# Kernel optimization log

Hardware: AMD Instinct MI355X
Metric: run time of the kernel (lower is better)

## Reference

```python
import jax, jax.numpy as jnp
import numpy as np

N, E = 50000, 800000
DIN, H, R, HEADS, DH, OUT = 256, 128, 8, 8, 16, 3  # DH = H // HEADS


def setup_inputs() -> dict:
    key = jax.random.key(0)
    ks = jax.random.split(key, 16)
    g = lambda k, shape, fan: jax.random.normal(k, shape, jnp.float32) * np.float32(np.sqrt(2.0 / fan))
    return {
        'x': jax.random.normal(ks[0], (N, DIN), jnp.float32),
        'edge_index': jax.random.randint(ks[1], (2, E), 0, N, jnp.int32),
        'edge_type': jax.random.randint(ks[2], (E,), 0, R, jnp.int32),
        'Wp': g(ks[3], (DIN, H), DIN), 'bp': jnp.zeros((H,), jnp.float32),
        'W1': g(ks[4], (R, H, H), H), 'root1': g(ks[5], (H, H), H), 'b1': jnp.zeros((H,), jnp.float32),
        'W2': g(ks[6], (R, H, H), H), 'root2': g(ks[7], (H, H), H), 'b2': jnp.zeros((H,), jnp.float32),
        'Wg': g(ks[8], (H, HEADS * DH), H), 'att': g(ks[9], (1, HEADS, 2 * DH), 2 * DH),
        'bg': jnp.zeros((HEADS * DH,), jnp.float32),
        'Wf': g(ks[10], (H, OUT), H), 'bf': jnp.zeros((OUT,), jnp.float32),
    }


def _rgcn(h, src, tgt, etype, W, root, b):
    # h: [N,H]; per-relation: mean-aggregate W_r @ h_src over edges of type r
    n = h.shape[0]
    h_src = h[src]                                   # [E,H]
    out = h @ root
    for r in range(R):
        mask = (etype == r)
        msg = jnp.where(mask[:, None], h_src @ W[r], 0.0)          # [E,H]
        agg = jax.ops.segment_sum(msg, tgt, num_segments=n)        # [N,H]
        deg = jax.ops.segment_sum(mask.astype(h.dtype), tgt, num_segments=n)
        out = out + agg / jnp.clip(deg, 1.0)[:, None]
    return out + b


def _gat(h, src, tgt, Wg, att, bg, negative_slope=0.2):
    n = h.shape[0]
    z = (h @ Wg).reshape(n, HEADS, DH)               # [N,heads,dh]
    z_src, z_tgt = z[src], z[tgt]                    # [E,heads,dh]
    alpha = (z_src * att[:, :, :DH]).sum(-1) + (z_tgt * att[:, :, DH:]).sum(-1)  # [E,heads]
    alpha = jax.nn.leaky_relu(alpha, negative_slope)
    amax = jax.ops.segment_max(alpha, tgt, num_segments=n)         # [N,heads]
    ex = jnp.exp(alpha - amax[tgt])
    denom = jnp.clip(jax.ops.segment_sum(ex, tgt, num_segments=n), 1e-16)
    alpha = ex / denom[tgt]
    out = jax.ops.segment_sum(z_src * alpha[:, :, None], tgt, num_segments=n)  # [N,heads,dh]
    return out.reshape(n, HEADS * DH) + bg


def reference(x, edge_index, edge_type, Wp, bp, W1, root1, b1, W2, root2, b2, Wg, att, bg, Wf, bf):
    src, tgt = edge_index[0], edge_index[1]
    h = x @ Wp + bp
    h = jax.nn.relu(_rgcn(h, src, tgt, edge_type, W1, root1, b1))
    h = jax.nn.relu(_rgcn(h, src, tgt, edge_type, W2, root2, b2))
    h = _gat(h, src, tgt, Wg, att, bg)
    logits = h @ Wf + bf
    return jax.nn.log_softmax(logits, axis=-1)
```

## Files before the change

kernel.cpp:

```cpp
#include <hip/hip_runtime.h>
#include <math.h>

#define NN      50000
#define EE      800000
#define DIN     256
#define HF      128
#define RR      8
#define NHEADS  8
#define DHH     16
#define OUTC    3
#define M2      (NN * RR)
#define NB2     ((M2 + 255) / 256)
#define CH2     ((NB2 + 255) / 256)

static inline int cdiv(long long a, int b) { return (int)((a + b - 1) / b); }

typedef __attribute__((ext_vector_type(8))) short short8;
typedef __attribute__((ext_vector_type(4))) float f32x4;

__device__ inline float bf2f(unsigned short u) {
    return __uint_as_float(((unsigned)u) << 16);
}
__device__ inline unsigned short f2bf(float f) {
    unsigned u = __float_as_uint(f);
    u += 0x7fffu + ((u >> 16) & 1u);
    return (unsigned short)(u >> 16);
}

__global__ __launch_bounds__(256) void prep_weights(const float* __restrict__ Wp,
                                                    const float* __restrict__ W1,
                                                    const float* __restrict__ root1,
                                                    const float* __restrict__ W2,
                                                    const float* __restrict__ root2,
                                                    const float* __restrict__ Wg,
                                                    unsigned short* __restrict__ Wtp_hi,
                                                    unsigned short* __restrict__ Wtp_lo,
                                                    unsigned short* __restrict__ Wt1_hi,
                                                    unsigned short* __restrict__ Wt1_lo,
                                                    unsigned short* __restrict__ Wt2_hi,
                                                    unsigned short* __restrict__ Wt2_lo,
                                                    unsigned short* __restrict__ Wtg_hi,
                                                    unsigned short* __restrict__ Wtg_lo) {
    int i = blockIdx.x * 256 + threadIdx.x;
    if (i >= 344064) return;
    const float* src; unsigned short *dh, *dl; int k0, ldk, base;
    if (i < 32768)       { src = Wp;    dh = Wtp_hi; dl = Wtp_lo; k0 = 0;    ldk = 256;  base = 0; }
    else if (i < 163840) { src = W1;    dh = Wt1_hi; dl = Wt1_lo; k0 = 0;    ldk = 1152; base = 32768; }
    else if (i < 180224) { src = root1; dh = Wt1_hi; dl = Wt1_lo; k0 = 1024; ldk = 1152; base = 163840; }
    else if (i < 311296) { src = W2;    dh = Wt2_hi; dl = Wt2_lo; k0 = 0;    ldk = 1152; base = 180224; }
    else if (i < 327680) { src = root2; dh = Wt2_hi; dl = Wt2_lo; k0 = 1024; ldk = 1152; base = 311296; }
    else                 { src = Wg;    dh = Wtg_hi; dl = Wtg_lo; k0 = 0;    ldk = 128;  base = 327680; }
    int j = i - base;
    int k = j >> 7, n = j & 127;
    float f = src[(size_t)k * 128 + n];
    unsigned short hi = f2bf(f);
    unsigned short lo = f2bf(f - bf2f(hi));
    dh[(size_t)n * ldk + k0 + k] = hi;
    dl[(size_t)n * ldk + k0 + k] = lo;
}

__global__ __launch_bounds__(256) void count2_kernel(const int* __restrict__ tgt,
                                                     const int* __restrict__ et,
                                                     int* __restrict__ cnt2) {
    int i = blockIdx.x * 256 + threadIdx.x;
    if (i < EE) atomicAdd(&cnt2[tgt[i] * RR + et[i]], 1);
}

__global__ __launch_bounds__(256) void scan1_kernel(const int* __restrict__ cnt,
                                                    int* __restrict__ bsum, int n) {
    __shared__ int s[256];
    int t = threadIdx.x;
    int i = blockIdx.x * 256 + t;
    s[t] = (i < n) ? cnt[i] : 0;
    __syncthreads();
    for (int off = 128; off > 0; off >>= 1) {
        if (t < off) s[t] += s[t + off];
        __syncthreads();
    }
    if (t == 0) bsum[blockIdx.x] = s[0];
}

__global__ __launch_bounds__(256) void scan2_kernel(const int* __restrict__ bsum,
                                                    int* __restrict__ bbase,
                                                    int* __restrict__ tail,
                                                    int nb, int ch) {
    __shared__ int s[256];
    int t = threadIdx.x;
    int beg = t * ch;
    int end = beg + ch; if (end > nb) end = nb;
    int sum = 0;
    for (int i = beg; i < end; i++) sum += bsum[i];
    s[t] = sum;
    __syncthreads();
    for (int off = 1; off < 256; off <<= 1) {
        int u = (t >= off) ? s[t - off] : 0;
        __syncthreads();
        s[t] += u;
        __syncthreads();
    }
    int run = s[t] - sum;
    for (int i = beg; i < end; i++) {
        bbase[i] = run;
        run += bsum[i];
    }
    if (t == 255) *tail = s[255];
}

__global__ __launch_bounds__(256) void scan3_kernel(const int* __restrict__ cnt,
                                                    const int* __restrict__ bbase,
                                                    int* __restrict__ rowptr,
                                                    int* __restrict__ cursor, int n) {
    __shared__ int s[256];
    int t = threadIdx.x;
    int i = blockIdx.x * 256 + t;
    int v = (i < n) ? cnt[i] : 0;
    s[t] = v;
    __syncthreads();
    for (int off = 1; off < 256; off <<= 1) {
        int u = (t >= off) ? s[t - off] : 0;
        __syncthreads();
        s[t] += u;
        __syncthreads();
    }
    if (i < n) {
        int e = bbase[blockIdx.x] + s[t] - v;
        rowptr[i] = e;
        cursor[i] = e;
    }
}

__global__ __launch_bounds__(256) void fill2_kernel(const int* __restrict__ src,
                                                    const int* __restrict__ tgt,
                                                    const int* __restrict__ et,
                                                    int* __restrict__ cursor2,
                                                    int* __restrict__ csr_src2) {
    int e = blockIdx.x * 256 + threadIdx.x;
    if (e >= EE) return;
    int pos = atomicAdd(&cursor2[tgt[e] * RR + et[e]], 1);
    csr_src2[pos] = src[e];
}

#define BK 32
#define APAD 36

template <bool SPLITA, bool ACC, bool BIAS, bool RELU, bool BF16OUT>
__global__ __launch_bounds__(256) void gemm_mfma(const void* __restrict__ Av, int lda,
                                                 const unsigned short* __restrict__ Bthi,
                                                 const unsigned short* __restrict__ Btlo, int ldk,
                                                 float* __restrict__ C,
                                                 unsigned short* __restrict__ Cb,
                                                 const float* __restrict__ bias,
                                                 int M, int K) {
    __shared__ unsigned short Ah[128 * APAD];
    __shared__ unsigned short Al[(SPLITA ? 128 : 1) * APAD];
    __shared__ unsigned short Bh[128 * APAD];
    __shared__ unsigned short Bl[128 * APAD];
    const int tid  = threadIdx.x;
    const int m0   = blockIdx.x * 128;
    const int w    = tid >> 6;
    const int lane = tid & 63;
    const int lrow = lane & 15;
    const int q    = lane >> 4;

    f32x4 acc[2][8];
#pragma unroll
    for (int t = 0; t < 2; t++)
#pragma unroll
        for (int c = 0; c < 8; c++) acc[t][c] = (f32x4){0.f, 0.f, 0.f, 0.f};

    const int srow  = tid >> 1;
    const int spart = (tid & 1) * 16;

    for (int k0 = 0; k0 < K; k0 += BK) {
        if (SPLITA) {
            const float* A = (const float*)Av;
            int gm = m0 + srow;
            float va[16];
            if (gm < M) {
                const float* ap = &A[(size_t)gm * lda + k0 + spart];
#pragma unroll
                for (int j = 0; j < 4; j++) {
                    float4 v = *reinterpret_cast<const float4*>(ap + j * 4);
                    va[j * 4 + 0] = v.x; va[j * 4 + 1] = v.y; va[j * 4 + 2] = v.z; va[j * 4 + 3] = v.w;
                }
            } else {
#pragma unroll
                for (int j = 0; j < 16; j++) va[j] = 0.f;
            }
            unsigned hw[8], lw[8];
#pragma unroll
            for (int j = 0; j < 8; j++) {
                unsigned short h0 = f2bf(va[2 * j]);
                unsigned short h1 = f2bf(va[2 * j + 1]);
                unsigned short l0 = f2bf(va[2 * j] - bf2f(h0));
                unsigned short l1 = f2bf(va[2 * j + 1] - bf2f(h1));
                hw[j] = (unsigned)h0 | ((unsigned)h1 << 16);
                lw[j] = (unsigned)l0 | ((unsigned)l1 << 16);
            }
            *reinterpret_cast<uint4*>(&Ah[srow * APAD + spart])     = make_uint4(hw[0], hw[1], hw[2], hw[3]);
            *reinterpret_cast<uint4*>(&Ah[srow * APAD + spart + 8]) = make_uint4(hw[4], hw[5], hw[6], hw[7]);
            *reinterpret_cast<uint4*>(&Al[srow * APAD + spart])     = make_uint4(lw[0], lw[1], lw[2], lw[3]);
            *reinterpret_cast<uint4*>(&Al[srow * APAD + spart + 8]) = make_uint4(lw[4], lw[5], lw[6], lw[7]);
        } else {
            const unsigned short* A = (const unsigned short*)Av;
            int gm = m0 + srow;
            uint4 v  = make_uint4(0u, 0u, 0u, 0u);
            uint4 v2 = make_uint4(0u, 0u, 0u, 0u);
            if (gm < M) {
                const unsigned short* ap = &A[(size_t)gm * lda + k0 + spart];
                v  = *reinterpret_cast<const uint4*>(ap);
                v2 = *reinterpret_cast<const uint4*>(ap + 8);
            }
            *reinterpret_cast<uint4*>(&Ah[srow * APAD + spart])     = v;
            *reinterpret_cast<uint4*>(&Ah[srow * APAD + spart + 8]) = v2;
        }
        {
            const unsigned short* bh = &Bthi[(size_t)srow * ldk + k0 + spart];
            const unsigned short* bl = &Btlo[(size_t)srow * ldk + k0 + spart];
            *reinterpret_cast<uint4*>(&Bh[srow * APAD + spart])     = *reinterpret_cast<const uint4*>(bh);
            *reinterpret_cast<uint4*>(&Bh[srow * APAD + spart + 8]) = *reinterpret_cast<const uint4*>(bh + 8);
            *reinterpret_cast<uint4*>(&Bl[srow * APAD + spart])     = *reinterpret_cast<const uint4*>(bl);
            *reinterpret_cast<uint4*>(&Bl[srow * APAD + spart + 8]) = *reinterpret_cast<const uint4*>(bl + 8);
        }
        __syncthreads();

        short8 ah[2], al[2];
#pragma unroll
        for (int t = 0; t < 2; t++) {
            ah[t] = *reinterpret_cast<const short8*>(&Ah[(w * 32 + t * 16 + lrow) * APAD + q * 8]);
            if (SPLITA)
                al[t] = *reinterpret_cast<const short8*>(&Al[(w * 32 + t * 16 + lrow) * APAD + q * 8]);
        }
#pragma unroll
        for (int c = 0; c < 8; c++) {
            short8 bh = *reinterpret_cast<const short8*>(&Bh[(c * 16 + lrow) * APAD + q * 8]);
            short8 bl = *reinterpret_cast<const short8*>(&Bl[(c * 16 + lrow) * APAD + q * 8]);
#pragma unroll
            for (int t = 0; t < 2; t++) {
                acc[t][c] = __builtin_amdgcn_mfma_f32_16x16x32_bf16(ah[t], bl, acc[t][c], 0, 0, 0);
                if (SPLITA)
                    acc[t][c] = __builtin_amdgcn_mfma_f32_16x16x32_bf16(al[t], bh, acc[t][c], 0, 0, 0);
                acc[t][c] = __builtin_amdgcn_mfma_f32_16x16x32_bf16(ah[t], bh, acc[t][c], 0, 0, 0);
            }
        }
        __syncthreads();
    }

#pragma unroll
    for (int t = 0; t < 2; t++) {
#pragma unroll
        for (int r = 0; r < 4; r++) {
            int gm = m0 + w * 32 + t * 16 + q * 4 + r;
            if (gm >= M) continue;
#pragma unroll
            for (int c = 0; c < 8; c++) {
                int gn = c * 16 + lrow;
                float v = acc[t][c][r];
                if (BIAS) v += bias[gn];
                if (ACC)  v += C[(size_t)gm * HF + gn];
                if (RELU) v = fmaxf(v, 0.f);
                C[(size_t)gm * HF + gn] = v;
                if (BF16OUT) Cb[(size_t)gm * HF + gn] = f2bf(v);
            }
        }
    }
}

__global__ __launch_bounds__(256) void gemm_rgcn(const unsigned short* __restrict__ aggb,
                                                 const float* __restrict__ hin,
                                                 const unsigned short* __restrict__ Bthi,
                                                 const unsigned short* __restrict__ Btlo,
                                                 float* __restrict__ hout,
                                                 unsigned short* __restrict__ hbout,
                                                 const float* __restrict__ bias, int M) {
    const int LDK = (RR + 1) * HF;
    __shared__ unsigned short Ah[128 * APAD];
    __shared__ unsigned short Al[128 * APAD];
    __shared__ unsigned short Bh[128 * APAD];
    __shared__ unsigned short Bl[128 * APAD];
    const int tid  = threadIdx.x;
    const int m0   = blockIdx.x * 128;
    const int w    = tid >> 6;
    const int lane = tid & 63;
    const int lrow = lane & 15;
    const int q    = lane >> 4;

    f32x4 acc[2][8];
#pragma unroll
    for (int t = 0; t < 2; t++)
#pragma unroll
        for (int c = 0; c < 8; c++) acc[t][c] = (f32x4){0.f, 0.f, 0.f, 0.f};

    const int srow  = tid >> 1;
    const int spart = (tid & 1) * 16;

    for (int k0 = 0; k0 < RR * HF; k0 += BK) {
        {
            int gm = m0 + srow;
            uint4 v  = make_uint4(0u, 0u, 0u, 0u);
            uint4 v2 = make_uint4(0u, 0u, 0u, 0u);
            if (gm < M) {
                const unsigned short* ap = &aggb[(size_t)gm * (RR * HF) + k0 + spart];
                v  = *reinterpret_cast<const uint4*>(ap);
                v2 = *reinterpret_cast<const uint4*>(ap + 8);
            }
            *reinterpret_cast<uint4*>(&Ah[srow * APAD + spart])     = v;
            *reinterpret_cast<uint4*>(&Ah[srow * APAD + spart + 8]) = v2;
        }
        {
            const unsigned short* bh = &Bthi[(size_t)srow * LDK + k0 + spart];
            const unsigned short* bl = &Btlo[(size_t)srow * LDK + k0 + spart];
            *reinterpret_cast<uint4*>(&Bh[srow * APAD + spart])     = *reinterpret_cast<const uint4*>(bh);
            *reinterpret_cast<uint4*>(&Bh[srow * APAD + spart + 8]) = *reinterpret_cast<const uint4*>(bh + 8);
            *reinterpret_cast<uint4*>(&Bl[srow * APAD + spart])     = *reinterpret_cast<const uint4*>(bl);
            *reinterpret_cast<uint4*>(&Bl[srow * APAD + spart + 8]) = *reinterpret_cast<const uint4*>(bl + 8);
        }
        __syncthreads();
        short8 ah[2];
#pragma unroll
        for (int t = 0; t < 2; t++)
            ah[t] = *reinterpret_cast<const short8*>(&Ah[(w * 32 + t * 16 + lrow) * APAD + q * 8]);
#pragma unroll
        for (int c = 0; c < 8; c++) {
            short8 bh = *reinterpret_cast<const short8*>(&Bh[(c * 16 + lrow) * APAD + q * 8]);
            short8 bl = *reinterpret_cast<const short8*>(&Bl[(c * 16 + lrow) * APAD + q * 8]);
#pragma unroll
            for (int t = 0; t < 2; t++) {
                acc[t][c] = __builtin_amdgcn_mfma_f32_16x16x32_bf16(ah[t], bl, acc[t][c], 0, 0, 0);
                acc[t][c] = __builtin_amdgcn_mfma_f32_16x16x32_bf16(ah[t], bh, acc[t][c], 0, 0, 0);
            }
        }
        __syncthreads();
    }

    for (int k0 = 0; k0 < HF; k0 += BK) {
        {
            int gm = m0 + srow;
            float va[16];
            if (gm < M) {
                const float* ap = &hin[(size_t)gm * HF + k0 + spart];
#pragma unroll
                for (int j = 0; j < 4; j++) {
                    float4 v = *reinterpret_cast<const float4*>(ap + j * 4);
                    va[j * 4 + 0] = v.x; va[j * 4 + 1] = v.y; va[j * 4 + 2] = v.z; va[j * 4 + 3] = v.w;
                }
            } else {
#pragma unroll
                for (int j = 0; j < 16; j++) va[j] = 0.f;
            }
            unsigned hw[8], lw[8];
#pragma unroll
            for (int j = 0; j < 8; j++) {
                unsigned short h0 = f2bf(va[2 * j]);
                unsigned short h1 = f2bf(va[2 * j + 1]);
                unsigned short l0 = f2bf(va[2 * j] - bf2f(h0));
                unsigned short l1 = f2bf(va[2 * j + 1] - bf2f(h1));
                hw[j] = (unsigned)h0 | ((unsigned)h1 << 16);
                lw[j] = (unsigned)l0 | ((unsigned)l1 << 16);
            }
            *reinterpret_cast<uint4*>(&Ah[srow * APAD + spart])     = make_uint4(hw[0], hw[1], hw[2], hw[3]);
            *reinterpret_cast<uint4*>(&Ah[srow * APAD + spart + 8]) = make_uint4(hw[4], hw[5], hw[6], hw[7]);
            *reinterpret_cast<uint4*>(&Al[srow * APAD + spart])     = make_uint4(lw[0], lw[1], lw[2], lw[3]);
            *reinterpret_cast<uint4*>(&Al[srow * APAD + spart + 8]) = make_uint4(lw[4], lw[5], lw[6], lw[7]);
        }
        {
            const unsigned short* bh = &Bthi[(size_t)srow * LDK + RR * HF + k0 + spart];
            const unsigned short* bl = &Btlo[(size_t)srow * LDK + RR * HF + k0 + spart];
            *reinterpret_cast<uint4*>(&Bh[srow * APAD + spart])     = *reinterpret_cast<const uint4*>(bh);
            *reinterpret_cast<uint4*>(&Bh[srow * APAD + spart + 8]) = *reinterpret_cast<const uint4*>(bh + 8);
            *reinterpret_cast<uint4*>(&Bl[srow * APAD + spart])     = *reinterpret_cast<const uint4*>(bl);
            *reinterpret_cast<uint4*>(&Bl[srow * APAD + spart + 8]) = *reinterpret_cast<const uint4*>(bl + 8);
        }
        __syncthreads();
        short8 ah[2], al[2];
#pragma unroll
        for (int t = 0; t < 2; t++) {
            ah[t] = *reinterpret_cast<const short8*>(&Ah[(w * 32 + t * 16 + lrow) * APAD + q * 8]);
            al[t] = *reinterpret_cast<const short8*>(&Al[(w * 32 + t * 16 + lrow) * APAD + q * 8]);
        }
#pragma unroll
        for (int c = 0; c < 8; c++) {
            short8 bh = *reinterpret_cast<const short8*>(&Bh[(c * 16 + lrow) * APAD + q * 8]);
            short8 bl = *reinterpret_cast<const short8*>(&Bl[(c * 16 + lrow) * APAD + q * 8]);
#pragma unroll
            for (int t = 0; t < 2; t++) {
                acc[t][c] = __builtin_amdgcn_mfma_f32_16x16x32_bf16(ah[t], bl, acc[t][c], 0, 0, 0);
                acc[t][c] = __builtin_amdgcn_mfma_f32_16x16x32_bf16(al[t], bh, acc[t][c], 0, 0, 0);
                acc[t][c] = __builtin_amdgcn_mfma_f32_16x16x32_bf16(ah[t], bh, acc[t][c], 0, 0, 0);
            }
        }
        __syncthreads();
    }

#pragma unroll
    for (int t = 0; t < 2; t++) {
#pragma unroll
        for (int r = 0; r < 4; r++) {
            int gm = m0 + w * 32 + t * 16 + q * 4 + r;
            if (gm >= M) continue;
#pragma unroll
            for (int c = 0; c < 8; c++) {
                int gn = c * 16 + lrow;
                float v = fmaxf(acc[t][c][r] + bias[gn], 0.f);
                hout[(size_t)gm * HF + gn] = v;
                hbout[(size_t)gm * HF + gn] = f2bf(v);
            }
        }
    }
}

__global__ __launch_bounds__(256) void gemm_z(const float* __restrict__ hin,
                                              const unsigned short* __restrict__ Bthi,
                                              const unsigned short* __restrict__ Btlo,
                                              const float* __restrict__ att,
                                              unsigned short* __restrict__ zb,
                                              float* __restrict__ a_src,
                                              float* __restrict__ a_tgt, int M) {
    __shared__ unsigned short Ah[128 * APAD];
    __shared__ unsigned short Al[128 * APAD];
    __shared__ unsigned short Bh[128 * APAD];
    __shared__ unsigned short Bl[128 * APAD];
    const int tid  = threadIdx.x;
    const int m0   = blockIdx.x * 128;
    const int w    = tid >> 6;
    const int lane = tid & 63;
    const int lrow = lane & 15;
    const int q    = lane >> 4;

    f32x4 acc[2][8];
#pragma unroll
    for (int t = 0; t < 2; t++)
#pragma unroll
        for (int c = 0; c < 8; c++) acc[t][c] = (f32x4){0.f, 0.f, 0.f, 0.f};

    const int srow  = tid >> 1;
    const int spart = (tid & 1) * 16;

    for (int k0 = 0; k0 < HF; k0 += BK) {
        {
            int gm = m0 + srow;
            float va[16];
            if (gm < M) {
                const float* ap = &hin[(size_t)gm * HF + k0 + spart];
#pragma unroll
                for (int j = 0; j < 4; j++) {
                    float4 v = *reinterpret_cast<const float4*>(ap + j * 4);
                    va[j * 4 + 0] = v.x; va[j * 4 + 1] = v.y; va[j * 4 + 2] = v.z; va[j * 4 + 3] = v.w;
                }
            } else {
#pragma unroll
                for (int j = 0; j < 16; j++) va[j] = 0.f;
            }
            unsigned hw[8], lw[8];
#pragma unroll
            for (int j = 0; j < 8; j++) {
                unsigned short h0 = f2bf(va[2 * j]);
                unsigned short h1 = f2bf(va[2 * j + 1]);
                unsigned short l0 = f2bf(va[2 * j] - bf2f(h0));
                unsigned short l1 = f2bf(va[2 * j + 1] - bf2f(h1));
                hw[j] = (unsigned)h0 | ((unsigned)h1 << 16);
                lw[j] = (unsigned)l0 | ((unsigned)l1 << 16);
            }
            *reinterpret_cast<uint4*>(&Ah[srow * APAD + spart])     = make_uint4(hw[0], hw[1], hw[2], hw[3]);
            *reinterpret_cast<uint4*>(&Ah[srow * APAD + spart + 8]) = make_uint4(hw[4], hw[5], hw[6], hw[7]);
            *reinterpret_cast<uint4*>(&Al[srow * APAD + spart])     = make_uint4(lw[0], lw[1], lw[2], lw[3]);
            *reinterpret_cast<uint4*>(&Al[srow * APAD + spart + 8]) = make_uint4(lw[4], lw[5], lw[6], lw[7]);
        }
        {
            const unsigned short* bh = &Bthi[(size_t)srow * HF + k0 + spart];
            const unsigned short* bl = &Btlo[(size_t)srow * HF + k0 + spart];
            *reinterpret_cast<uint4*>(&Bh[srow * APAD + spart])     = *reinterpret_cast<const uint4*>(bh);
            *reinterpret_cast<uint4*>(&Bh[srow * APAD + spart + 8]) = *reinterpret_cast<const uint4*>(bh + 8);
            *reinterpret_cast<uint4*>(&Bl[srow * APAD + spart])     = *reinterpret_cast<const uint4*>(bl);
            *reinterpret_cast<uint4*>(&Bl[srow * APAD + spart + 8]) = *reinterpret_cast<const uint4*>(bl + 8);
        }
        __syncthreads();
        short8 ah[2], al[2];
#pragma unroll
        for (int t = 0; t < 2; t++) {
            ah[t] = *reinterpret_cast<const short8*>(&Ah[(w * 32 + t * 16 + lrow) * APAD + q * 8]);
            al[t] = *reinterpret_cast<const short8*>(&Al[(w * 32 + t * 16 + lrow) * APAD + q * 8]);
        }
#pragma unroll
        for (int c = 0; c < 8; c++) {
            short8 bh = *reinterpret_cast<const short8*>(&Bh[(c * 16 + lrow) * APAD + q * 8]);
            short8 bl = *reinterpret_cast<const short8*>(&Bl[(c * 16 + lrow) * APAD + q * 8]);
#pragma unroll
            for (int t = 0; t < 2; t++) {
                acc[t][c] = __builtin_amdgcn_mfma_f32_16x16x32_bf16(ah[t], bl, acc[t][c], 0, 0, 0);
                acc[t][c] = __builtin_amdgcn_mfma_f32_16x16x32_bf16(al[t], bh, acc[t][c], 0, 0, 0);
                acc[t][c] = __builtin_amdgcn_mfma_f32_16x16x32_bf16(ah[t], bh, acc[t][c], 0, 0, 0);
            }
        }
        __syncthreads();
    }

    float att_s[8], att_t[8];
#pragma unroll
    for (int c = 0; c < 8; c++) {
        att_s[c] = att[c * 32 + lrow];
        att_t[c] = att[c * 32 + 16 + lrow];
    }

#pragma unroll
    for (int t = 0; t < 2; t++) {
#pragma unroll
        for (int r = 0; r < 4; r++) {
            int gm = m0 + w * 32 + t * 16 + q * 4 + r;
            if (gm >= M) continue;
#pragma unroll
            for (int c = 0; c < 8; c++) {
                int gn = c * 16 + lrow;
                float v = acc[t][c][r];
                zb[(size_t)gm * HF + gn] = f2bf(v);
                float ps = v * att_s[c];
                float pt = v * att_t[c];
#pragma unroll
                for (int off = 1; off < 16; off <<= 1) {
                    ps += __shfl_xor(ps, off);
                    pt += __shfl_xor(pt, off);
                }
                if (lrow == 0) {
                    a_src[(size_t)gm * NHEADS + c] = ps;
                    a_tgt[(size_t)gm * NHEADS + c] = pt;
                }
            }
        }
    }
}

__global__ __launch_bounds__(256) void rgcn_agg_sorted(const unsigned short* __restrict__ hb,
                                                       const int* __restrict__ rowptr2,
                                                       const int* __restrict__ csr_src2,
                                                       unsigned short* __restrict__ agg) {
    int w = (blockIdx.x * 256 + threadIdx.x) >> 6;
    if (w >= NN) return;
    int lane = threadIdx.x & 63;
    int half = lane >> 5;
    int c4 = (lane & 31) * 4;
    const int b8 = w * RR;
    unsigned short* o = &agg[(size_t)w * (RR * HF)];
    int b = rowptr2[b8];
#pragma unroll
    for (int r = 0; r < RR; r++) {
        int e2 = rowptr2[b8 + r + 1];
        float a0 = 0.f, a1 = 0.f, a2 = 0.f, a3 = 0.f;
        for (int e = b + half; e < e2; e += 2) {
            int s = csr_src2[e];
            uint2 v = *reinterpret_cast<const uint2*>(&hb[(size_t)s * HF + c4]);
            a0 += bf2f((unsigned short)(v.x & 0xffffu));
            a1 += bf2f((unsigned short)(v.x >> 16));
            a2 += bf2f((unsigned short)(v.y & 0xffffu));
            a3 += bf2f((unsigned short)(v.y >> 16));
        }
        a0 += __shfl_xor(a0, 32);
        a1 += __shfl_xor(a1, 32);
        a2 += __shfl_xor(a2, 32);
        a3 += __shfl_xor(a3, 32);
        int n = e2 - b;
        float inv = 1.f / (float)(n > 1 ? n : 1);
        if (half == 0) {
            uint2 p;
            p.x = (unsigned)f2bf(a0 * inv) | ((unsigned)f2bf(a1 * inv) << 16);
            p.y = (unsigned)f2bf(a2 * inv) | ((unsigned)f2bf(a3 * inv) << 16);
            *reinterpret_cast<uint2*>(&o[r * HF + c4]) = p;
        }
        b = e2;
    }
}

__global__ __launch_bounds__(256) void gat_kernel(const int* __restrict__ rowptr2,
                                                  const int* __restrict__ csr_src2,
                                                  const float* __restrict__ a_src,
                                                  const float* __restrict__ a_tgt,
                                                  const unsigned short* __restrict__ zb,
                                                  const float* __restrict__ bg,
                                                  const float* __restrict__ Wf,
                                                  const float* __restrict__ bf,
                                                  float* __restrict__ out) {
    int w = (blockIdx.x * 256 + threadIdx.x) >> 6;
    if (w >= NN) return;
    int lane = threadIdx.x & 63;
    int beg = rowptr2[w * RR], end = rowptr2[w * RR + RR];

    int hdA = lane & 7;
    int e8  = lane >> 3;
    float atA = a_tgt[w * NHEADS + hdA];
    float m = -1e30f;
    for (int e = beg + e8; e < end; e += 8) {
        int s = csr_src2[e];
        float a = a_src[s * NHEADS + hdA] + atA;
        a = a > 0.f ? a : 0.2f * a;
        m = fmaxf(m, a);
    }
    m = fmaxf(m, __shfl_xor(m, 8));
    m = fmaxf(m, __shfl_xor(m, 16));
    m = fmaxf(m, __shfl_xor(m, 32));

    int hd = lane >> 3;
    int c0 = lane * 2;
    float mB = __shfl(m, hd);
    float at = __shfl(atA, hd);
    float l0 = 0.f, l1 = 0.f;
    float ax0 = 0.f, ay0 = 0.f, ax1 = 0.f, ay1 = 0.f;
    int e = beg;
    for (; e + 1 < end; e += 2) {
        int s0 = csr_src2[e], s1 = csr_src2[e + 1];
        float a0 = a_src[s0 * NHEADS + hd] + at;
        float a1 = a_src[s1 * NHEADS + hd] + at;
        a0 = a0 > 0.f ? a0 : 0.2f * a0;
        a1 = a1 > 0.f ? a1 : 0.2f * a1;
        float w0 = __expf(a0 - mB);
        float w1 = __expf(a1 - mB);
        unsigned z0 = *reinterpret_cast<const unsigned*>(&zb[(size_t)s0 * HF + c0]);
        unsigned z1 = *reinterpret_cast<const unsigned*>(&zb[(size_t)s1 * HF + c0]);
        l0 += w0; l1 += w1;
        ax0 += bf2f((unsigned short)(z0 & 0xffffu)) * w0;
        ay0 += bf2f((unsigned short)(z0 >> 16)) * w0;
        ax1 += bf2f((unsigned short)(z1 & 0xffffu)) * w1;
        ay1 += bf2f((unsigned short)(z1 >> 16)) * w1;
    }
    if (e < end) {
        int s0 = csr_src2[e];
        float a0 = a_src[s0 * NHEADS + hd] + at;
        a0 = a0 > 0.f ? a0 : 0.2f * a0;
        float w0 = __expf(a0 - mB);
        unsigned z0 = *reinterpret_cast<const unsigned*>(&zb[(size_t)s0 * HF + c0]);
        l0 += w0;
        ax0 += bf2f((unsigned short)(z0 & 0xffffu)) * w0;
        ay0 += bf2f((unsigned short)(z0 >> 16)) * w0;
    }
    float l = l0 + l1;
    float ax = ax0 + ax1, ay = ay0 + ay1;

    float inv = 1.f / fmaxf(l, 1e-16f);
    float vx = ax * inv + bg[c0];
    float vy = ay * inv + bg[c0 + 1];

    float p0 = vx * Wf[c0 * 3 + 0] + vy * Wf[(c0 + 1) * 3 + 0];
    float p1 = vx * Wf[c0 * 3 + 1] + vy * Wf[(c0 + 1) * 3 + 1];
    float p2 = vx * Wf[c0 * 3 + 2] + vy * Wf[(c0 + 1) * 3 + 2];
#pragma unroll
    for (int off = 32; off > 0; off >>= 1) {
        p0 += __shfl_xor(p0, off);
        p1 += __shfl_xor(p1, off);
        p2 += __shfl_xor(p2, off);
    }
    if (lane == 0) {
        float l0v = p0 + bf[0], l1v = p1 + bf[1], l2v = p2 + bf[2];
        float mm = fmaxf(l0v, fmaxf(l1v, l2v));
        float lse = mm + logf(expf(l0v - mm) + expf(l1v - mm) + expf(l2v - mm));
        out[(size_t)w * 3 + 0] = l0v - lse;
        out[(size_t)w * 3 + 1] = l1v - lse;
        out[(size_t)w * 3 + 2] = l2v - lse;
    }
}

extern "C" void kernel_launch(void* const* d_in, const int* in_sizes, int n_in,
                              void* d_out, int out_size, void* d_ws, size_t ws_size,
                              hipStream_t stream) {
    const float* x     = (const float*)d_in[0];
    const int*   ei    = (const int*)d_in[1];
    const int*   etype = (const int*)d_in[2];
    const float* Wp    = (const float*)d_in[3];
    const float* bp    = (const float*)d_in[4];
    const float* W1    = (const float*)d_in[5];
    const float* root1 = (const float*)d_in[6];
    const float* b1    = (const float*)d_in[7];
    const float* W2    = (const float*)d_in[8];
    const float* root2 = (const float*)d_in[9];
    const float* b2    = (const float*)d_in[10];
    const float* Wg    = (const float*)d_in[11];
    const float* att   = (const float*)d_in[12];
    const float* bg    = (const float*)d_in[13];
    const float* Wf    = (const float*)d_in[14];
    const float* bf    = (const float*)d_in[15];
    (void)in_sizes; (void)n_in; (void)out_size; (void)ws_size;

    const int* srcv = ei;
    const int* tgtv = ei + EE;

    char* base = (char*)d_ws;
    unsigned short* aggb = (unsigned short*)(base + 0);
    int* cnt2    = (int*)(base + 96000000);
    int* cursor2 = (int*)(base + 98000000);
    int* bsum2   = (int*)(base + 99700000);
    int* bbase2  = (int*)(base + 99800000);
    unsigned short* zb = (unsigned short*)(base + 0);
    float* a_src = (float*)(base + 12800000);
    float* a_tgt = (float*)(base + 14400000);
    float* h1    = (float*)(base + 102400000);
    float* h2    = (float*)(base + 128000000);
    unsigned short* h1b = (unsigned short*)(base + 153600000);
    unsigned short* h2b = (unsigned short*)(base + 166400000);
    int* csr_src2 = (int*)(base + 179200000);
    int* rowptr2  = (int*)(base + 182400000);
    unsigned short* Wtp_hi = (unsigned short*)(base + 184000016);
    unsigned short* Wtp_lo = (unsigned short*)(base + 184065552);
    unsigned short* Wt1_hi = (unsigned short*)(base + 184131088);
    unsigned short* Wt1_lo = (unsigned short*)(base + 184426000);
    unsigned short* Wt2_hi = (unsigned short*)(base + 184720912);
    unsigned short* Wt2_lo = (unsigned short*)(base + 185015824);
    unsigned short* Wtg_hi = (unsigned short*)(base + 185310736);
    unsigned short* Wtg_lo = (unsigned short*)(base + 185343504);

    prep_weights<<<cdiv(344064, 256), 256, 0, stream>>>(
        Wp, W1, root1, W2, root2, Wg,
        Wtp_hi, Wtp_lo, Wt1_hi, Wt1_lo, Wt2_hi, Wt2_lo, Wtg_hi, Wtg_lo);

    hipMemsetAsync(cnt2, 0, (size_t)M2 * 4, stream);
    count2_kernel<<<cdiv(EE, 256), 256, 0, stream>>>(tgtv, etype, cnt2);
    scan1_kernel<<<NB2, 256, 0, stream>>>(cnt2, bsum2, M2);
    scan2_kernel<<<1, 256, 0, stream>>>(bsum2, bbase2, &rowptr2[M2], NB2, CH2);
    scan3_kernel<<<NB2, 256, 0, stream>>>(cnt2, bbase2, rowptr2, cursor2, M2);
    fill2_kernel<<<cdiv(EE, 256), 256, 0, stream>>>(srcv, tgtv, etype, cursor2, csr_src2);

    const int ggrid  = cdiv(NN, 128);
    const int nwgrid = cdiv(NN, 4);

    gemm_mfma<true, false, true, false, true><<<ggrid, 256, 0, stream>>>(
        x, DIN, Wtp_hi, Wtp_lo, DIN, h1, h1b, bp, NN, DIN);

    rgcn_agg_sorted<<<nwgrid, 256, 0, stream>>>(h1b, rowptr2, csr_src2, aggb);
    gemm_rgcn<<<ggrid, 256, 0, stream>>>(aggb, h1, Wt1_hi, Wt1_lo, h2, h2b, b1, NN);

    rgcn_agg_sorted<<<nwgrid, 256, 0, stream>>>(h2b, rowptr2, csr_src2, aggb);
    gemm_rgcn<<<ggrid, 256, 0, stream>>>(aggb, h2, Wt2_hi, Wt2_lo, h1, h1b, b2, NN);

    gemm_z<<<ggrid, 256, 0, stream>>>(h1, Wtg_hi, Wtg_lo, att, zb, a_src, a_tgt, NN);
    gat_kernel<<<nwgrid, 256, 0, stream>>>(rowptr2, csr_src2, a_src, a_tgt, zb, bg, Wf, bf, (float*)d_out);
}
```

Before: 594.2 us.

## Process all relations in parallel per wave in RGCN aggregation

The RGCN mean-aggregation kernel now gives each of the 8 relations its own group of 8 lanes within the wave, with each lane covering 16 features through two 16-byte loads. Previously the kernel looped over relations one after another, with half-waves splitting the edges. The new layout removes the serial relation loop and the cross-half shuffle reduction, and unrolls the edge loop by two to keep more loads in flight. In exchange, lanes see unequal work when relations have different edge counts, and each lane holds more registers.

```diff
diff --git a/kernel.cpp b/kernel.cpp
--- a/kernel.cpp
+++ b/kernel.cpp
@@ -529,6 +529,17 @@
     }
 }
 
+__device__ inline void acc8(float* a, uint4 v) {
+    a[0] += bf2f((unsigned short)(v.x & 0xffffu));
+    a[1] += bf2f((unsigned short)(v.x >> 16));
+    a[2] += bf2f((unsigned short)(v.y & 0xffffu));
+    a[3] += bf2f((unsigned short)(v.y >> 16));
+    a[4] += bf2f((unsigned short)(v.z & 0xffffu));
+    a[5] += bf2f((unsigned short)(v.z >> 16));
+    a[6] += bf2f((unsigned short)(v.w & 0xffffu));
+    a[7] += bf2f((unsigned short)(v.w >> 16));
+}
+
 __global__ __launch_bounds__(256) void rgcn_agg_sorted(const unsigned short* __restrict__ hb,
                                                        const int* __restrict__ rowptr2,
                                                        const int* __restrict__ csr_src2,
@@ -536,37 +547,52 @@
     int w = (blockIdx.x * 256 + threadIdx.x) >> 6;
     if (w >= NN) return;
     int lane = threadIdx.x & 63;
-    int half = lane >> 5;
-    int c4 = (lane & 31) * 4;
-    const int b8 = w * RR;
-    unsigned short* o = &agg[(size_t)w * (RR * HF)];
-    int b = rowptr2[b8];
-#pragma unroll
-    for (int r = 0; r < RR; r++) {
-        int e2 = rowptr2[b8 + r + 1];
-        float a0 = 0.f, a1 = 0.f, a2 = 0.f, a3 = 0.f;
-        for (int e = b + half; e < e2; e += 2) {
-            int s = csr_src2[e];
-            uint2 v = *reinterpret_cast<const uint2*>(&hb[(size_t)s * HF + c4]);
-            a0 += bf2f((unsigned short)(v.x & 0xffffu));
-            a1 += bf2f((unsigned short)(v.x >> 16));
-            a2 += bf2f((unsigned short)(v.y & 0xffffu));
-            a3 += bf2f((unsigned short)(v.y >> 16));
-        }
-        a0 += __shfl_xor(a0, 32);
-        a1 += __shfl_xor(a1, 32);
-        a2 += __shfl_xor(a2, 32);
-        a3 += __shfl_xor(a3, 32);
-        int n = e2 - b;
-        float inv = 1.f / (float)(n > 1 ? n : 1);
-        if (half == 0) {
-            uint2 p;
-            p.x = (unsigned)f2bf(a0 * inv) | ((unsigned)f2bf(a1 * inv) << 16);
-            p.y = (unsigned)f2bf(a2 * inv) | ((unsigned)f2bf(a3 * inv) << 16);
-            *reinterpret_cast<uint2*>(&o[r * HF + c4]) = p;
-        }
-        b = e2;
-    }
+    int r    = lane >> 3;
+    int cg   = (lane & 7) * 16;
+    int b8   = w * RR;
+
+    int rp  = rowptr2[b8 + (lane < 9 ? lane : 8)];
+    int beg = __shfl(rp, r);
+    int end = __shfl(rp, r + 1);
+
+    float a[16];
+#pragma unroll
+    for (int j = 0; j < 16; j++) a[j] = 0.f;
+
+    int e = beg;
+    for (; e + 1 < end; e += 2) {
+        int s0 = csr_src2[e];
+        int s1 = csr_src2[e + 1];
+        const uint4* p0 = reinterpret_cast<const uint4*>(&hb[(size_t)s0 * HF + cg]);
+        const uint4* p1 = reinterpret_cast<const uint4*>(&hb[(size_t)s1 * HF + cg]);
+        uint4 v00 = p0[0];
+        uint4 v01 = p0[1];
+        uint4 v10 = p1[0];
+        uint4 v11 = p1[1];
+        acc8(a,     v00);
+        acc8(a + 8, v01);
+        acc8(a,     v10);
+        acc8(a + 8, v11);
+    }
+    if (e < end) {
+        int s0 = csr_src2[e];
+        const uint4* p0 = reinterpret_cast<const uint4*>(&hb[(size_t)s0 * HF + cg]);
+        uint4 v00 = p0[0];
+        uint4 v01 = p0[1];
+        acc8(a,     v00);
+        acc8(a + 8, v01);
+    }
+
+    int n = end - beg;
+    float inv = 1.f / (float)(n > 1 ? n : 1);
+    unsigned ow[8];
+#pragma unroll
+    for (int j = 0; j < 8; j++) {
+        ow[j] = (unsigned)f2bf(a[2 * j] * inv) | ((unsigned)f2bf(a[2 * j + 1] * inv) << 16);
+    }
+    unsigned short* o = &agg[(size_t)w * (RR * HF) + r * HF + cg];
+    *reinterpret_cast<uint4*>(o)     = make_uint4(ow[0], ow[1], ow[2], ow[3]);
+    *reinterpret_cast<uint4*>(o + 8) = make_uint4(ow[4], ow[5], ow[6], ow[7]);
 }
 
 __global__ __launch_bounds__(256) void gat_kernel(const int* __restrict__ rowptr2,
```

Result: faster. 525.7 us (-11.5%).
